# Performance work log

Hardware: AMD Instinct MI355X
Metric: run time of the kernel (lower is better)

The kernel has to match this reference:

```python
import jax, jax.numpy as jnp
import numpy as np

H, L, P, D_MODEL = 8, 4, 4, 256
HD = D_MODEL // H
SPATIAL = np.array([[100, 100], [50, 50], [25, 25], [13, 13]], dtype=np.int64)  # (h, w) per level


def _bilinear_sample(feat, gx, gy, lh, lw):
    """Bilinear sampling matching torch.F.grid_sample(align_corners=False, padding_mode='zeros').
    feat: [BH, lh*lw, D]; gx, gy: [BH, Nq, P] pixel coords. Returns [BH, Nq, P, D]."""
    x0 = jnp.floor(gx); y0 = jnp.floor(gy)
    wx = gx - x0; wy = gy - y0

    def gather(xf, yf):
        xi = xf.astype(jnp.int32); yi = yf.astype(jnp.int32)
        valid = (xi >= 0) & (xi < lw) & (yi >= 0) & (yi < lh)
        idx = jnp.clip(yi, 0, lh - 1) * lw + jnp.clip(xi, 0, lw - 1)
        BH = feat.shape[0]
        v = jnp.take_along_axis(feat, idx.reshape(BH, -1)[:, :, None], axis=1)
        v = v.reshape(xi.shape + (feat.shape[-1],))
        return v * valid[..., None].astype(feat.dtype)

    return (gather(x0, y0) * ((1 - wx) * (1 - wy))[..., None]
            + gather(x0 + 1, y0) * (wx * (1 - wy))[..., None]
            + gather(x0, y0 + 1) * ((1 - wx) * wy)[..., None]
            + gather(x0 + 1, y0 + 1) * (wx * wy)[..., None])


def _msda(query, reference_points, value, sp_np, Wso, bso, Waw, baw, Wv, bv, Wo, bo):
    B, Nq, _ = query.shape
    Nv = value.shape[1]
    v = (value @ Wv + bv).reshape(B, Nv, H, HD)  # value_proj
    off = (query @ Wso + bso).reshape(B, Nq, H, L, P, 2)  # sampling_offsets
    wh = jnp.asarray(sp_np[:, ::-1].copy(), jnp.float32)  # (w, h) per level
    loc = reference_points[:, :, None, :, None, :] + off / wh[None, None, None, :, None, :]
    grid = 2.0 * loc - 1.0  # [B, Nq, H, L, P, 2] in [-1, 1]
    aw = jax.nn.softmax((query @ Waw + baw).reshape(B, Nq, H, L * P), axis=-1).reshape(B, Nq, H, L, P)
    starts = np.concatenate([[0], np.cumsum(sp_np[:, 0] * sp_np[:, 1])]).astype(np.int64)
    out = jnp.zeros((B, H, Nq, HD), dtype=query.dtype)
    for lid in range(L):
        lh, lw = int(sp_np[lid, 0]), int(sp_np[lid, 1])
        feat = v[:, starts[lid]:starts[lid + 1]].transpose(0, 2, 1, 3).reshape(B * H, lh * lw, HD)
        g = grid[:, :, :, lid].transpose(0, 2, 1, 3, 4).reshape(B * H, Nq, P, 2)
        # align_corners=False: x_pix = ((gx + 1) * W - 1) / 2
        gx = (g[..., 0] + 1.0) * (lw * 0.5) - 0.5
        gy = (g[..., 1] + 1.0) * (lh * 0.5) - 0.5
        samp = _bilinear_sample(feat, gx, gy, lh, lw)  # [B*H, Nq, P, HD]
        w_l = aw[:, :, :, lid].transpose(0, 2, 1, 3).reshape(B * H, Nq, P)
        out = out + (samp * w_l[..., None]).sum(axis=2).reshape(B, H, Nq, HD)
    out = out.transpose(0, 2, 1, 3).reshape(B, Nq, D_MODEL)
    return out @ Wo + bo  # output_proj


def setup_inputs() -> dict:
    key = jax.random.key(0)
    ks = jax.random.split(key, 12)
    B, Nq = 2, int(np.sum(SPATIAL[:, 0] * SPATIAL[:, 1]))  # encoder: Nq == Nv == 13294
    Nv = Nq
    s = 1.0 / np.sqrt(D_MODEL).astype(np.float32)
    return {
        "query": jax.random.normal(ks[0], (B, Nq, D_MODEL), jnp.float32),
        "reference_points": jax.random.uniform(ks[1], (B, Nq, L, 2), dtype=jnp.float32),
        "value": jax.random.normal(ks[2], (B, Nv, D_MODEL), jnp.float32),
        "spatial_shapes": jnp.asarray(SPATIAL),
        "Wso": jax.random.normal(ks[3], (D_MODEL, H * L * P * 2), jnp.float32) * 0.01,
        "bso": jax.random.normal(ks[4], (H * L * P * 2,), jnp.float32) * 0.5,
        "Waw": jax.random.normal(ks[5], (D_MODEL, H * L * P), jnp.float32) * 0.01,
        "baw": jnp.zeros((H * L * P,), jnp.float32),
        "Wv": jax.random.normal(ks[6], (D_MODEL, D_MODEL), jnp.float32) * s,
        "bv": jnp.zeros((D_MODEL,), jnp.float32),
        "Wo": jax.random.normal(ks[7], (D_MODEL, D_MODEL), jnp.float32) * s,
        "bo": jnp.zeros((D_MODEL,), jnp.float32),
    }


def reference(query, reference_points, value, spatial_shapes, Wso, bso, Waw, baw, Wv, bv, Wo, bo):
    sp_np = np.asarray(spatial_shapes)  # static level shapes
    return _msda(query, reference_points, value, sp_np, Wso, bso, Waw, baw, Wv, bv, Wo, bo)
```

## Files before the change

kernel.cpp:

```cpp
#include <hip/hip_runtime.h>
#include <hip/hip_bf16.h>
#include <hip/hip_fp16.h>

typedef short s16x8 __attribute__((ext_vector_type(8)));
typedef float f32x4 __attribute__((ext_vector_type(4)));
typedef float f32x2 __attribute__((ext_vector_type(2)));
typedef unsigned int u32x4 __attribute__((ext_vector_type(4)));
typedef unsigned int u32x2 __attribute__((ext_vector_type(2)));

constexpr int Bb = 2, NQ = 13294, Hh = 8, HD = 32;
constexpr int Mrows = Bb * NQ;

__device__ inline short bf16_of(float f) {
  __hip_bfloat16 h = __float2bfloat16(f);
  return *reinterpret_cast<short*>(&h);
}

__global__ __launch_bounds__(256) void prep_k(
    const float* __restrict__ Wv, const float* __restrict__ Wso,
    const float* __restrict__ Waw, const float* __restrict__ Wo,
    const float* __restrict__ bso, const float* __restrict__ baw,
    short* __restrict__ WvT, short* __restrict__ WqT, short* __restrict__ WoT,
    float* __restrict__ bq)
{
  __shared__ short lds[64][65];
  const int tid = threadIdx.x;
  int t = blockIdx.x;
  if (t == 56) {
#pragma unroll
    for (int i = 0; i < 2; i++) {
      int id = i * 256 + tid;
      if (id < 384) bq[id] = id < 256 ? bso[id] : baw[id - 256];
    }
    return;
  }
  const float* src; short* dst; int ldS, n0, k0, drow0;
  if (t < 16)      { src = Wv;  dst = WvT; ldS = 256; n0 = (t >> 2) * 64;        k0 = (t & 3) * 64; drow0 = n0; }
  else if (t < 32) { t -= 16; src = Wso; dst = WqT; ldS = 256; n0 = (t >> 2) * 64; k0 = (t & 3) * 64; drow0 = n0; }
  else if (t < 40) { t -= 32; src = Waw; dst = WqT; ldS = 128; n0 = (t >> 2) * 64; k0 = (t & 3) * 64; drow0 = 256 + n0; }
  else             { t -= 40; src = Wo;  dst = WoT; ldS = 256; n0 = (t >> 2) * 64; k0 = (t & 3) * 64; drow0 = n0; }

#pragma unroll
  for (int i = 0; i < 16; i++) {
    int idx = i * 256 + tid;
    int kk = idx >> 6, nn = idx & 63;
    lds[nn][kk] = bf16_of(src[(size_t)(k0 + kk) * ldS + n0 + nn]);
  }
  __syncthreads();
#pragma unroll
  for (int i = 0; i < 16; i++) {
    int idx = i * 256 + tid;
    int nn = idx >> 6, kk = idx & 63;
    dst[(size_t)(drow0 + nn) * 256 + k0 + kk] = lds[nn][kk];
  }
}

template<int MODE>
__device__ __forceinline__ void gemm_body(
    const void* __restrict__ Araw, const short* __restrict__ WT,
    const float* __restrict__ bias, void* __restrict__ outraw,
    int wg, short (* __restrict__ As)[128][40], short (* __restrict__ Bs)[64][40])
{
  constexpr int NT = (MODE == 1) ? 6 : 4;
  const int xcd = wg & 7, local = wg >> 3;
  const int row0 = (xcd * 26 + local / NT) * 128;
  const int col0 = (local % NT) * 64;
  const int tid = threadIdx.x, lane = tid & 63, wave = tid >> 6;

  f32x4 acc[2][4] = {};

  int arow[2], aq[2], ga[2];
#pragma unroll
  for (int it = 0; it < 2; it++) {
    int task = it * 256 + tid;
    arow[it] = task >> 2; aq[it] = task & 3;
    ga[it] = min(row0 + arow[it], Mrows - 1);
  }
  const int bcol = tid >> 2, bqd = tid & 3;

  f32x4 a0[2], a1[2]; s16x8 abf[2]; s16x8 breg;

  auto load_tile = [&](int kt) {
#pragma unroll
    for (int it = 0; it < 2; it++) {
      if constexpr (MODE == 3) {
        abf[it] = *(const s16x8*)((const short*)Araw + (size_t)ga[it] * 256 + kt + aq[it] * 8);
      } else {
        const float* A = (const float*)Araw;
        a0[it] = *(const f32x4*)(A + (size_t)ga[it] * 256 + kt + aq[it] * 8);
        a1[it] = *(const f32x4*)(A + (size_t)ga[it] * 256 + kt + aq[it] * 8 + 4);
      }
    }
    breg = *(const s16x8*)(WT + (size_t)(col0 + bcol) * 256 + kt + bqd * 8);
  };

  auto write_tile = [&](int buf) {
#pragma unroll
    for (int it = 0; it < 2; it++) {
      s16x8 av;
      if constexpr (MODE == 3) { av = abf[it]; }
      else {
#pragma unroll
        for (int i = 0; i < 4; i++) { av[i] = bf16_of(a0[it][i]); av[4 + i] = bf16_of(a1[it][i]); }
      }
      *(s16x8*)(&As[buf][arow[it]][aq[it] * 8]) = av;
    }
    *(s16x8*)(&Bs[buf][bcol][bqd * 8]) = breg;
  };

  load_tile(0);
  const int fr = lane & 15, kg = lane >> 4;
#pragma unroll
  for (int t = 0; t < 8; t++) {
    const int buf = t & 1;
    write_tile(buf);
    __syncthreads();
    if (t < 7) load_tile((t + 1) * 32);
    s16x8 bfr[4], afr[2];
#pragma unroll
    for (int n = 0; n < 4; n++) bfr[n] = *(const s16x8*)(&Bs[buf][n * 16 + fr][kg * 8]);
#pragma unroll
    for (int m = 0; m < 2; m++) afr[m] = *(const s16x8*)(&As[buf][wave * 32 + m * 16 + fr][kg * 8]);
#pragma unroll
    for (int m = 0; m < 2; m++)
#pragma unroll
      for (int n = 0; n < 4; n++)
        acc[m][n] = __builtin_amdgcn_mfma_f32_16x16x32_bf16(afr[m], bfr[n], acc[m][n], 0, 0, 0);
  }

#pragma unroll
  for (int n = 0; n < 4; n++) {
    const int colL = col0 + n * 16 + fr;
    const float bvf = bias[colL];
#pragma unroll
    for (int m = 0; m < 2; m++) {
#pragma unroll
      for (int r = 0; r < 4; r++) {
        const int rowL = row0 + wave * 32 + m * 16 + kg * 4 + r;
        if (rowL < Mrows) {
          float v = acc[m][n][r] + bvf;
          if constexpr (MODE == 0) {
            int b = rowL >= NQ, nn = rowL - b * NQ;
            int h = colL >> 5, c = colL & 31;
            ((__half*)outraw)[(((size_t)b * Hh + h) * NQ + nn) * HD + c] = __float2half(v);
          } else if constexpr (MODE == 1) {
            ((__hip_bfloat16*)outraw)[(size_t)rowL * 384 + colL] = __float2bfloat16(v);
          } else {
            ((float*)outraw)[(size_t)rowL * 256 + colL] = v;
          }
        }
      }
    }
  }
}

__global__ __launch_bounds__(256) void gemm01_k(
    const float* __restrict__ value, const float* __restrict__ query,
    const short* __restrict__ WvT, const short* __restrict__ WqT,
    const float* __restrict__ bv, const float* __restrict__ bq,
    __half* __restrict__ vproj, __hip_bfloat16* __restrict__ offaw)
{
  __shared__ short As[2][128][40];
  __shared__ short Bs[2][64][40];
  const int wg = blockIdx.x;
  if (wg < 832) gemm_body<0>(value, WvT, bv, vproj, wg, As, Bs);
  else          gemm_body<1>(query, WqT, bq, offaw, wg - 832, As, Bs);
}

__global__ __launch_bounds__(256) void gemm3_k(
    const short* __restrict__ interm, const short* __restrict__ WoT,
    const float* __restrict__ bo, float* __restrict__ out)
{
  __shared__ short As[2][128][40];
  __shared__ short Bs[2][64][40];
  gemm_body<3>(interm, WoT, bo, out, blockIdx.x, As, Bs);
}

__global__ __launch_bounds__(256, 8) void sample_k(
    const __half* __restrict__ vproj,
    const __hip_bfloat16* __restrict__ offaw,
    const float* __restrict__ refp,
    __hip_bfloat16* __restrict__ interm)
{
  __shared__ u32x2 dpk[16][2][65];
  const int plane = blockIdx.x & 15;
  const int chunk = blockIdx.x >> 4;
  const int b = plane >> 3, h = plane & 7;
  const int q0 = chunk * 64;
  const int tid = threadIdx.x;
  const int wv = tid >> 6, lane = tid & 63;
  const int dims[4]   = {100, 50, 25, 13};
  const int starts[4] = {0, 10000, 12500, 13125};

#pragma unroll
  for (int it = 0; it < 4; it++) {
    const int ql = wv * 16 + it * 4 + (lane >> 4);
    const int lp = lane & 15;
    const int l = lp >> 2;
    const int lw = dims[l];
    int q = q0 + ql; if (q >= NQ) q = NQ - 1;
    const size_t row = (size_t)b * NQ + q;
    unsigned int oxy = *(const unsigned int*)((const unsigned short*)offaw + row * 384 + h * 32 + lp * 2);
    float offx = __uint_as_float(oxy << 16);
    float offy = __uint_as_float(oxy & 0xffff0000u);
    float logit = __bfloat162float(offaw[row * 384 + 256 + h * 16 + lp]);
    float2 rp = *(const float2*)(refp + (row * 4 + l) * 2);
    float gx = rp.x * (float)lw + offx - 0.5f;
    float gy = rp.y * (float)lw + offy - 0.5f;
    float e = __expf(logit);
    float ssum = e;
#pragma unroll
    for (int d = 1; d < 16; d <<= 1) ssum += __shfl_xor(ssum, d);
    float aw = e / ssum;

    float xf = floorf(gx), yf = floorf(gy);
    int x0 = (int)xf, y0 = (int)yf;
    float wx = gx - xf, wy = gy - yf;
    int bx = min(max(x0, 0), lw - 2);
    bool lxv = (x0 >= 0) & (x0 < lw);
    bool rxv = (x0 + 1 >= 0) & (x0 + 1 < lw);
    float wl = 1.f - wx, wr = wx;
    float ws0 = (lxv && x0 == bx     ? wl : 0.f) + (rxv && x0 + 1 == bx     ? wr : 0.f);
    float ws1 = (lxv && x0 == bx + 1 ? wl : 0.f) + (rxv && x0 + 1 == bx + 1 ? wr : 0.f);
    const int pbase = (b * Hh + h) * NQ + starts[l];
#pragma unroll
    for (int yi = 0; yi < 2; yi++) {
      int yc = y0 + yi;
      bool yv = (yc >= 0) & (yc < lw);
      int ycl = min(max(yc, 0), lw - 1);
      float wyt = (yi ? wy : 1.f - wy) * aw * (yv ? 1.f : 0.f);
      __half h0 = __float2half(ws0 * wyt);
      __half h1 = __float2half(ws1 * wyt);
      u32x2 pk;
      pk[0] = (unsigned int)((pbase + ycl * lw + bx) << 6);
      pk[1] = (unsigned int)(*(unsigned short*)&h0)
            | ((unsigned int)(*(unsigned short*)&h1) << 16);
      dpk[lp][yi][ql] = pk;
    }
  }
  asm volatile("s_waitcnt lgkmcnt(0)" ::: "memory");

  const int qh8 = lane >> 3;
  const int c8  = lane & 7;
  const int shsel = (c8 & 4) << 2;
  const int coff = c8 * 16;
#pragma unroll
  for (int half = 0; half < 2; half++) {
    const int ql = wv * 16 + half * 8 + qh8;
    __half2 acc2[4] = {};
#pragma unroll 4
    for (int lp = 0; lp < 16; lp++) {
#pragma unroll
      for (int yi = 0; yi < 2; yi++) {
        const u32x2 d = dpk[lp][yi][ql];
        const u32x4 u = *(const u32x4*)((const char*)vproj + d[0] + coff);
        unsigned short hw = (unsigned short)((d[1] >> shsel) & 0xffffu);
        __half2 ww = __half2half2(*(const __half*)&hw);
#pragma unroll
        for (int j = 0; j < 4; j++) {
          unsigned int t0 = u[j];
          acc2[j] = __hfma2(*reinterpret_cast<__half2*>(&t0), ww, acc2[j]);
        }
      }
    }
    float2 f[4];
#pragma unroll
    for (int j = 0; j < 4; j++) {
      f[j] = __half22float2(acc2[j]);
      f[j].x += __shfl_xor(f[j].x, 4);
      f[j].y += __shfl_xor(f[j].y, 4);
    }
    const int q = q0 + ql;
    if (c8 < 4 && q < NQ) {
      unsigned int up[4];
#pragma unroll
      for (int j = 0; j < 4; j++) {
        unsigned int b0 = (unsigned int)(unsigned short)bf16_of(f[j].x);
        unsigned int b1 = (unsigned int)(unsigned short)bf16_of(f[j].y);
        up[j] = (b1 << 16) | b0;
      }
      u32x4 pk = { up[0], up[1], up[2], up[3] };
      *(u32x4*)((unsigned short*)interm + ((size_t)b * NQ + q) * 256 + h * 32 + c8 * 8) = pk;
    }
  }
}

extern "C" void kernel_launch(void* const* d_in, const int* in_sizes, int n_in,
                              void* d_out, int out_size, void* d_ws, size_t ws_size,
                              hipStream_t stream)
{
  const float* query = (const float*)d_in[0];
  const float* refp  = (const float*)d_in[1];
  const float* value = (const float*)d_in[2];
  const float* Wso = (const float*)d_in[4];
  const float* bso = (const float*)d_in[5];
  const float* Waw = (const float*)d_in[6];
  const float* baw = (const float*)d_in[7];
  const float* Wv  = (const float*)d_in[8];
  const float* bv  = (const float*)d_in[9];
  const float* Wo  = (const float*)d_in[10];
  const float* bo  = (const float*)d_in[11];

  char* ws = (char*)d_ws;
  __half* vproj          = (__half*)ws;
  __hip_bfloat16* offaw  = (__hip_bfloat16*)(ws + 13613056);
  __hip_bfloat16* interm = (__hip_bfloat16*)(ws + 34032640);
  short* WvT = (short*)(ws + 47645696);
  short* WqT = (short*)(ws + 47776768);
  short* WoT = (short*)(ws + 47973376);
  float* bq  = (float*)(ws + 48104448);
  float* out = (float*)d_out;

  dim3 blk(256);
  prep_k<<<dim3(57), blk, 0, stream>>>(Wv, Wso, Waw, Wo, bso, baw, WvT, WqT, WoT, bq);
  gemm01_k<<<dim3(832 + 1248), blk, 0, stream>>>(value, query, WvT, WqT, bv, bq, vproj, offaw);
  sample_k<<<dim3(16 * 208), blk, 0, stream>>>(vproj, offaw, refp, interm);
  gemm3_k<<<dim3(832), blk, 0, stream>>>((const short*)interm, WoT, bo, out);
}
```

Baseline: 89.06 us.

## Stage GEMM tiles via direct global-to-LDS loads with XOR swizzle

Replaces the register-staged GEMM tile loads (global→VGPR→convert→LDS) with global_load_lds 16-byte async copies into an XOR-swizzled double buffer. Waits are handled by explicit vmcnt counts and raw barriers. For the fp32 operands, the A tile now sits in LDS as fp32 and is converted to bf16 when fragments are read, which doubles the A LDS footprint (40KB per block) and may reduce occupancy. Bias loads are hoisted ahead of the main loop.

```diff
diff --git a/kernel.cpp b/kernel.cpp
--- a/kernel.cpp
+++ b/kernel.cpp
@@ -4,7 +4,6 @@
 
 typedef short s16x8 __attribute__((ext_vector_type(8)));
 typedef float f32x4 __attribute__((ext_vector_type(4)));
-typedef float f32x2 __attribute__((ext_vector_type(2)));
 typedef unsigned int u32x4 __attribute__((ext_vector_type(4)));
 typedef unsigned int u32x2 __attribute__((ext_vector_type(2)));
 
@@ -14,6 +13,12 @@
 __device__ inline short bf16_of(float f) {
   __hip_bfloat16 h = __float2bfloat16(f);
   return *reinterpret_cast<short*>(&h);
+}
+
+__device__ __forceinline__ void gload16(const void* g, void* l) {
+  __builtin_amdgcn_global_load_lds(
+      (const __attribute__((address_space(1))) unsigned int*)g,
+      (__attribute__((address_space(3))) unsigned int*)l, 16, 0, 0);
 }
 
 __global__ __launch_bounds__(256) void prep_k(
@@ -59,68 +64,102 @@
 __device__ __forceinline__ void gemm_body(
     const void* __restrict__ Araw, const short* __restrict__ WT,
     const float* __restrict__ bias, void* __restrict__ outraw,
-    int wg, short (* __restrict__ As)[128][40], short (* __restrict__ Bs)[64][40])
+    int wg, char* __restrict__ ldsA, char* __restrict__ ldsB)
 {
   constexpr int NT = (MODE == 1) ? 6 : 4;
+  constexpr int ABYTES = (MODE == 3) ? 8192 : 16384;
   const int xcd = wg & 7, local = wg >> 3;
   const int row0 = (xcd * 26 + local / NT) * 128;
   const int col0 = (local % NT) * 64;
   const int tid = threadIdx.x, lane = tid & 63, wave = tid >> 6;
+  const int fr = lane & 15, kg = lane >> 4;
+
+  float bvf[4];
+#pragma unroll
+  for (int n = 0; n < 4; n++) bvf[n] = bias[col0 + n * 16 + fr];
+  asm volatile("" :: "v"(bvf[0]), "v"(bvf[1]), "v"(bvf[2]), "v"(bvf[3]));
+
+  const int rowB = tid >> 2, slB = (tid & 3) ^ (rowB & 3);
+  const short* srcB = WT + (size_t)(col0 + rowB) * 256 + slB * 8;
+  const int ldoffB = tid * 16;
+
+  const float* srcAf[4]; const short* srcAs[2]; int ldoffA[4];
+  if constexpr (MODE == 3) {
+#pragma unroll
+    for (int i = 0; i < 2; i++) {
+      int rowA = i * 64 + (tid >> 2);
+      int rowc = min(row0 + rowA, Mrows - 1);
+      int slA = (tid & 3) ^ (rowA & 3);
+      srcAs[i] = (const short*)Araw + (size_t)rowc * 256 + slA * 8;
+      ldoffA[i] = i * 4096 + tid * 16;
+    }
+  } else {
+#pragma unroll
+    for (int i = 0; i < 4; i++) {
+      int rowA = i * 32 + (tid >> 3);
+      int rowc = min(row0 + rowA, Mrows - 1);
+      int slA = (tid & 7) ^ (rowA & 7);
+      srcAf[i] = (const float*)Araw + (size_t)rowc * 256 + slA * 4;
+      ldoffA[i] = i * 4096 + tid * 16;
+    }
+  }
+
+  auto stage = [&](int bufsel, int kt) {
+    char* Ab = ldsA + bufsel * ABYTES;
+    char* Bd = ldsB + bufsel * 4096;
+    if constexpr (MODE == 3) {
+#pragma unroll
+      for (int i = 0; i < 2; i++) gload16(srcAs[i] + kt, Ab + ldoffA[i]);
+    } else {
+#pragma unroll
+      for (int i = 0; i < 4; i++) gload16(srcAf[i] + kt, Ab + ldoffA[i]);
+    }
+    gload16(srcB + kt, Bd + ldoffB);
+  };
 
   f32x4 acc[2][4] = {};
-
-  int arow[2], aq[2], ga[2];
-#pragma unroll
-  for (int it = 0; it < 2; it++) {
-    int task = it * 256 + tid;
-    arow[it] = task >> 2; aq[it] = task & 3;
-    ga[it] = min(row0 + arow[it], Mrows - 1);
-  }
-  const int bcol = tid >> 2, bqd = tid & 3;
-
-  f32x4 a0[2], a1[2]; s16x8 abf[2]; s16x8 breg;
-
-  auto load_tile = [&](int kt) {
-#pragma unroll
-    for (int it = 0; it < 2; it++) {
-      if constexpr (MODE == 3) {
-        abf[it] = *(const s16x8*)((const short*)Araw + (size_t)ga[it] * 256 + kt + aq[it] * 8);
-      } else {
-        const float* A = (const float*)Araw;
-        a0[it] = *(const f32x4*)(A + (size_t)ga[it] * 256 + kt + aq[it] * 8);
-        a1[it] = *(const f32x4*)(A + (size_t)ga[it] * 256 + kt + aq[it] * 8 + 4);
-      }
-    }
-    breg = *(const s16x8*)(WT + (size_t)(col0 + bcol) * 256 + kt + bqd * 8);
-  };
-
-  auto write_tile = [&](int buf) {
-#pragma unroll
-    for (int it = 0; it < 2; it++) {
-      s16x8 av;
-      if constexpr (MODE == 3) { av = abf[it]; }
-      else {
-#pragma unroll
-        for (int i = 0; i < 4; i++) { av[i] = bf16_of(a0[it][i]); av[4 + i] = bf16_of(a1[it][i]); }
-      }
-      *(s16x8*)(&As[buf][arow[it]][aq[it] * 8]) = av;
-    }
-    *(s16x8*)(&Bs[buf][bcol][bqd * 8]) = breg;
-  };
-
-  load_tile(0);
-  const int fr = lane & 15, kg = lane >> 4;
+  stage(0, 0);
+
 #pragma unroll
   for (int t = 0; t < 8; t++) {
     const int buf = t & 1;
-    write_tile(buf);
-    __syncthreads();
-    if (t < 7) load_tile((t + 1) * 32);
-    s16x8 bfr[4], afr[2];
-#pragma unroll
-    for (int n = 0; n < 4; n++) bfr[n] = *(const s16x8*)(&Bs[buf][n * 16 + fr][kg * 8]);
-#pragma unroll
-    for (int m = 0; m < 2; m++) afr[m] = *(const s16x8*)(&As[buf][wave * 32 + m * 16 + fr][kg * 8]);
+    if (t < 7) {
+      stage(buf ^ 1, (t + 1) * 32);
+      if constexpr (MODE == 3) asm volatile("s_waitcnt vmcnt(3)" ::: "memory");
+      else                     asm volatile("s_waitcnt vmcnt(5)" ::: "memory");
+    } else {
+      asm volatile("s_waitcnt vmcnt(0)" ::: "memory");
+    }
+    __builtin_amdgcn_s_barrier();
+
+    const char* Ab = ldsA + buf * ABYTES;
+    const char* Bd = ldsB + buf * 4096;
+    s16x8 afr[2], bfr[4];
+#pragma unroll
+    for (int m = 0; m < 2; m++) {
+      const int row = wave * 32 + m * 16 + fr;
+      if constexpr (MODE == 3) {
+        const int slot = kg ^ (row & 3);
+        afr[m] = *(const s16x8*)(Ab + row * 64 + slot * 16);
+      } else {
+        const int s0 = (2 * kg) ^ (row & 7);
+        const f32x4 lo = *(const f32x4*)(Ab + row * 128 + s0 * 16);
+        const f32x4 hi = *(const f32x4*)(Ab + row * 128 + (s0 ^ 1) * 16);
+        s16x8 av;
+#pragma unroll
+        for (int i = 0; i < 4; i++) { av[i] = bf16_of(lo[i]); av[4 + i] = bf16_of(hi[i]); }
+        afr[m] = av;
+      }
+    }
+#pragma unroll
+    for (int n = 0; n < 4; n++) {
+      const int row = n * 16 + fr;
+      const int slot = kg ^ (row & 3);
+      bfr[n] = *(const s16x8*)(Bd + row * 64 + slot * 16);
+    }
+    asm volatile("s_waitcnt lgkmcnt(0)" ::: "memory");
+    __builtin_amdgcn_s_barrier();
+
 #pragma unroll
     for (int m = 0; m < 2; m++)
 #pragma unroll
@@ -131,14 +170,13 @@
 #pragma unroll
   for (int n = 0; n < 4; n++) {
     const int colL = col0 + n * 16 + fr;
-    const float bvf = bias[colL];
 #pragma unroll
     for (int m = 0; m < 2; m++) {
 #pragma unroll
       for (int r = 0; r < 4; r++) {
         const int rowL = row0 + wave * 32 + m * 16 + kg * 4 + r;
         if (rowL < Mrows) {
-          float v = acc[m][n][r] + bvf;
+          float v = acc[m][n][r] + bvf[n];
           if constexpr (MODE == 0) {
             int b = rowL >= NQ, nn = rowL - b * NQ;
             int h = colL >> 5, c = colL & 31;
@@ -160,20 +198,22 @@
     const float* __restrict__ bv, const float* __restrict__ bq,
     __half* __restrict__ vproj, __hip_bfloat16* __restrict__ offaw)
 {
-  __shared__ short As[2][128][40];
-  __shared__ short Bs[2][64][40];
+  __shared__ __align__(16) char lds[40960];
+  char* ldsA = lds;
+  char* ldsB = lds + 32768;
   const int wg = blockIdx.x;
-  if (wg < 832) gemm_body<0>(value, WvT, bv, vproj, wg, As, Bs);
-  else          gemm_body<1>(query, WqT, bq, offaw, wg - 832, As, Bs);
+  if (wg < 832) gemm_body<0>(value, WvT, bv, vproj, wg, ldsA, ldsB);
+  else          gemm_body<1>(query, WqT, bq, offaw, wg - 832, ldsA, ldsB);
 }
 
 __global__ __launch_bounds__(256) void gemm3_k(
     const short* __restrict__ interm, const short* __restrict__ WoT,
     const float* __restrict__ bo, float* __restrict__ out)
 {
-  __shared__ short As[2][128][40];
-  __shared__ short Bs[2][64][40];
-  gemm_body<3>(interm, WoT, bo, out, blockIdx.x, As, Bs);
+  __shared__ __align__(16) char lds[24576];
+  char* ldsA = lds;
+  char* ldsB = lds + 16384;
+  gemm_body<3>(interm, WoT, bo, out, blockIdx.x, ldsA, ldsB);
 }
 
 __global__ __launch_bounds__(256, 8) void sample_k(
```

Measured after the change: 80.90 us. 1.1x faster.
